# Performance work log

Measured on AMD Instinct MI355X. Metric: run time of the kernel, lower is better.

## Reference

```python
import jax, jax.numpy as jnp
import numpy as np

B, T, CIN, CH, SZ = 4, 6, 3, 64, 128
KS = [3, 5, 7]


def _conv(x, w, b, pad):
    # x: [N,Ci,H,W], w: [Co,Ci,k,k]
    y = jax.lax.conv_general_dilated(
        x, w, window_strides=(1, 1), padding=[(pad, pad), (pad, pad)],
        dimension_numbers=('NCHW', 'OIHW', 'NCHW'))
    return y + b[None, :, None, None]


def setup_inputs() -> dict:
    key = jax.random.key(0)
    ks = jax.random.split(key, 16)
    inp = {}
    inp['x'] = jax.random.normal(ks[0], (B, T, CIN, SZ, SZ), jnp.float32)
    for i in range(3):
        inp[f'h{i}'] = jnp.zeros((B, CH, SZ, SZ), jnp.float32)
    # 1x1 projection conv
    inp['w1x1'] = jax.random.normal(ks[1], (CH, CIN, 1, 1), jnp.float32) / np.sqrt(CIN).astype(np.float32)
    inp['b1x1'] = jnp.zeros((CH,), jnp.float32)
    # 3 ConvGRU layers, gates: reset (r), update (u), out (o)
    ki = 2
    for i, k in enumerate(KS):
        cin = (CIN if i == 0 else CH) + CH  # concat(input, hidden)
        s = np.float32(1.0 / np.sqrt(cin * k * k))
        for g in ('r', 'u', 'o'):
            inp[f'w{g}{i}'] = jax.random.normal(ks[ki], (CH, cin, k, k), jnp.float32) * s
            inp[f'b{g}{i}'] = jnp.zeros((CH,), jnp.float32)
            ki += 1
    return inp


def _cell(inp, h, wr, br, wu, bu, wo, bo, k):
    pad = k // 2
    stacked = jnp.concatenate([inp, h], axis=1)
    u = jax.nn.sigmoid(_conv(stacked, wu, bu, pad))
    r = jax.nn.sigmoid(_conv(stacked, wr, br, pad))
    o = jnp.tanh(_conv(jnp.concatenate([inp, h * r], axis=1), wo, bo, pad))
    return h * (1.0 - u) + o * u


def reference(x, h0, h1, h2, w1x1, b1x1,
              wr0, br0, wu0, bu0, wo0, bo0,
              wr1, br1, wu1, bu1, wo1, bo1,
              wr2, br2, wu2, bu2, wo2, bo2):
    b, t, c, hh, ww = x.shape
    x0 = _conv(x.reshape(b * t, c, hh, ww), w1x1, b1x1, 0)  # [b*t, CH, H, W]
    layers = [(wr0, br0, wu0, bu0, wo0, bo0, 3),
              (wr1, br1, wu1, bu1, wo1, bo1, 5),
              (wr2, br2, wu2, bu2, wo2, bo2, 7)]

    def step(carry, xt):
        hs = list(carry)
        layer_in = xt
        new_hs = []
        for i, (wr, br, wu, bu, wo, bo, k) in enumerate(layers):
            hn = _cell(layer_in, hs[i], wr, br, wu, bu, wo, bo, k)
            new_hs.append(hn)
            layer_in = hn
        return tuple(new_hs), None

    xs = jnp.transpose(x, (1, 0, 2, 3, 4))  # [t,b,c,H,W]
    (h0f, h1f, h2f), _ = jax.lax.scan(step, (h0, h1, h2), xs)
    # original returns ((x0, hidden[-1]), hidden); flattened here
    return (x0, h0f, h1f, h2f)
```

## Files before the change

### kernel.cpp

```cpp
#include <hip/hip_runtime.h>
#include <math.h>

constexpr int Bn  = 4;
constexpr int T   = 6;
constexpr int CIN = 3;
constexpr int CH  = 64;
constexpr int IMG = 128;
constexpr int HW  = IMG * IMG;

constexpr int CLY = 136;
constexpr long CLN = 4L * CLY * CLY * 64;
constexpr long CLNX = 4L * CLY * CLY * 32;

typedef short bf16x8 __attribute__((ext_vector_type(8)));
typedef float f32x4  __attribute__((ext_vector_type(4)));

__device__ __forceinline__ unsigned short f2bf(float f) {
    union { float f; unsigned int u; } v; v.f = f;
    unsigned int u = v.u;
    unsigned int r = (u + 0x7FFFu + ((u >> 16) & 1u)) >> 16;
    return (unsigned short)r;
}
__device__ __forceinline__ float bf2f(unsigned short s) {
    union { unsigned int u; float f; } v; v.u = ((unsigned int)s) << 16;
    return v.f;
}
__device__ __forceinline__ float sigmoidf_(float v) { return 1.f / (1.f + __expf(-v)); }
__device__ __forceinline__ float tanhf_(float v)    { return 1.f - 2.f / (1.f + __expf(2.f * v)); }

__global__ void xform_w(const float* __restrict__ wA, const float* __restrict__ wB,
                        unsigned short* __restrict__ dst,
                        int K, int C0, int NCIC, int NG) {
    int idx   = blockIdx.x * 256 + threadIdx.x;
    int total = NG * K * K * NCIC * 4 * 64;
    if (idx >= total) return;
    int CI   = C0 + 64;
    int KK   = K * K;
    int lane = idx & 63;
    int rest = idx >> 6;
    int c    = rest & 3; rest >>= 2;
    int cic  = rest % NCIC; rest /= NCIC;
    int kyx  = rest % KK;
    int cog  = rest / KK;
    const float* w = cog ? wB : wA;
    int co = c * 16 + (lane & 15);
    union { unsigned short u[8]; uint4 q; } t;
    #pragma unroll
    for (int j = 0; j < 8; ++j) {
        int ci_new = cic * 32 + ((lane >> 4) * 8) + j;
        int ci_o   = (ci_new < 64) ? (C0 + ci_new) : (ci_new - 64);
        bool valid = (ci_new < 64) || (ci_new - 64 < C0);
        float f = valid ? w[((long)co * CI + ci_o) * KK + kyx] : 0.f;
        t.u[j] = f2bf(f);
    }
    *(uint4*)(dst + (long)(idx >> 6) * 8 * 64 + lane * 8) = t.q;
}

__global__ void build_cl(const float* __restrict__ src, long bstride, int C0,
                         unsigned short* __restrict__ dst, int NG, int CST) {
    int i    = blockIdx.x * 256 + threadIdx.x;
    int px   = i & 16383;
    int rest = i >> 14;
    int g    = rest % NG;
    int b    = rest / NG;
    int y    = px >> 7, x = px & 127;
    union { unsigned short u[8]; uint4 q; } t;
    #pragma unroll
    for (int j = 0; j < 8; ++j) {
        int ci  = g * 8 + j;
        float f = (ci < C0) ? src[(long)b * bstride + (long)ci * HW + px] : 0.f;
        t.u[j] = f2bf(f);
    }
    long off = (((long)b * CLY + 4 + y) * CLY + 4 + x) * CST + g * 8;
    *(uint4*)(dst + off) = t.q;
}

__global__ void unpack_h(const unsigned short* __restrict__ clh, float* __restrict__ H) {
    int i  = blockIdx.x * 256 + threadIdx.x;
    int b  = i >> 14, px = i & 16383;
    int y  = px >> 7, x = px & 127;
    const unsigned short* p = clh + (((long)b * CLY + 4 + y) * CLY + 4 + x) * 64;
    float* Hb = H + (long)b * 64 * HW + px;
    #pragma unroll
    for (int g = 0; g < 8; ++g) {
        union { unsigned short us[8]; uint4 q; } t;
        t.q = *(const uint4*)(p + g * 8);
        #pragma unroll
        for (int j = 0; j < 8; ++j)
            Hb[(long)(g * 8 + j) * HW] = bf2f(t.us[j]);
    }
}

template<int K, int NCIC, int S, int MODE, int CST>
__global__ __launch_bounds__(256)
void conv_l0(const unsigned short* __restrict__ clh,
             const unsigned short* __restrict__ clin,
             const unsigned short* __restrict__ wt,
             const float* __restrict__ bias_a,
             const float* __restrict__ bias_b,
             unsigned short* __restrict__ ubuf,
             unsigned short* __restrict__ clh2,
             unsigned short* __restrict__ clhL)
{
    constexpr int HOFF = 4 - K / 2;
    constexpr int KK   = K * K;
    constexpr int NF   = NCIC * 4;
    __shared__ unsigned short alds[2][NF * 512];

    int w    = threadIdx.x >> 6;
    int lane = threadIdx.x & 63;
    int cog  = (MODE == 0) ? blockIdx.y : 0;
    int m    = blockIdx.x;
    int k8   = m & 7;
    int q    = m >> 3;
    int b    = k8 >> 1;
    int y, x0;
    if (S == 4) { y = (k8 & 1) * 64 + (q >> 1) * 4 + w; x0 = (q & 1) * 64; }
    else        { y = (k8 & 1) * 64 + (q >> 2) * 4 + w; x0 = (q & 3) * 32; }
    int n  = lane & 15;
    int kg = lane >> 4;

    f32x4 acc[4][S];
    #pragma unroll
    for (int c = 0; c < 4; ++c)
        #pragma unroll
        for (int s = 0; s < S; ++s)
            acc[c][s] = (f32x4){0.f, 0.f, 0.f, 0.f};

    long rbh = ((long)(b * CLY + HOFF + y) * CLY + HOFF + x0 + n) * 64 + kg * 8;
    long rbi = ((long)(b * CLY + HOFF + y) * CLY + HOFF + x0 + n) * CST + kg * 8;
    const unsigned short* wcog = wt + (long)cog * KK * NF * 512;

    #define STAGEW(bi, kyx_) do {                                              \
        const unsigned short* _src = wcog + (long)(kyx_) * NF * 512;           \
        _Pragma("unroll")                                                      \
        for (int j = 0; j < NCIC; ++j) {                                       \
            int f = j * 4 + w;                                                 \
            __builtin_amdgcn_global_load_lds(                                  \
                (const __attribute__((address_space(1))) void*)(_src + f * 512 + lane * 8), \
                (__attribute__((address_space(3))) void*)(&alds[bi][f * 512]), \
                16, 0, 0);                                                     \
        }                                                                      \
    } while (0)

    STAGEW(0, 0);
    int cur = 0;
    for (int kyx = 0; kyx < KK; ++kyx) {
        if (kyx + 1 < KK) {
            STAGEW(cur ^ 1, kyx + 1);
            asm volatile("s_waitcnt vmcnt(%0)" :: "n"(NCIC) : "memory");
        } else {
            asm volatile("s_waitcnt vmcnt(0)" ::: "memory");
        }
        __builtin_amdgcn_s_barrier();
        asm volatile("" ::: "memory");

        int ky = kyx / K;
        int kx = kyx - ky * K;
        long offh = rbh + (long)(ky * CLY + kx) * 64;
        long offi = rbi + (long)(ky * CLY + kx) * CST;
        #pragma unroll
        for (int cic = 0; cic < NCIC; ++cic) {
            bf16x8 bfr[S], afr[4];
            #pragma unroll
            for (int s = 0; s < S; ++s) {
                if (cic < 2) bfr[s] = *(const bf16x8*)(clh  + offh + s * 16 * 64  + cic * 32);
                else         bfr[s] = *(const bf16x8*)(clin + offi + s * 16 * CST + (cic - 2) * 32);
            }
            #pragma unroll
            for (int c = 0; c < 4; ++c)
                afr[c] = *(const bf16x8*)(&alds[cur][(cic * 4 + c) * 512 + lane * 8]);
            #pragma unroll
            for (int c = 0; c < 4; ++c)
                #pragma unroll
                for (int s = 0; s < S; ++s)
                    acc[c][s] = __builtin_amdgcn_mfma_f32_16x16x32_bf16(afr[c], bfr[s], acc[c][s], 0, 0, 0);
        }
        asm volatile("" ::: "memory");
        __builtin_amdgcn_s_barrier();
        cur ^= 1;
    }
    #undef STAGEW

    #pragma unroll
    for (int coc = 0; coc < 4; ++coc) {
        int co_l = coc * 16 + kg * 4;
        #pragma unroll
        for (int s = 0; s < S; ++s) {
            int x = x0 + s * 16 + n;
            f32x4 v = acc[coc][s];
            long cloff = (((long)b * CLY + 4 + y) * CLY + 4 + x) * 64 + co_l;
            if (MODE == 0) {
                if (cog == 0) {
                    union { unsigned short us[4]; unsigned long long d; } t;
                    #pragma unroll
                    for (int rr = 0; rr < 4; ++rr)
                        t.us[rr] = f2bf(sigmoidf_(v[rr] + bias_a[co_l + rr]));
                    *(unsigned long long*)(ubuf + (((long)b * HW + y * IMG + x) * 64 + co_l)) = t.d;
                } else {
                    union { unsigned short us[4]; unsigned long long d; } hh, t;
                    hh.d = *(const unsigned long long*)(clh + cloff);
                    #pragma unroll
                    for (int rr = 0; rr < 4; ++rr) {
                        float rv = sigmoidf_(v[rr] + bias_b[co_l + rr]);
                        t.us[rr] = f2bf(bf2f(hh.us[rr]) * rv);
                    }
                    *(unsigned long long*)(clh2 + cloff) = t.d;
                }
            } else {
                union { unsigned short us[4]; unsigned long long d; } uu, hh, t;
                uu.d = *(const unsigned long long*)(ubuf + (((long)b * HW + y * IMG + x) * 64 + co_l));
                hh.d = *(const unsigned long long*)(clhL + cloff);
                #pragma unroll
                for (int rr = 0; rr < 4; ++rr) {
                    float o  = tanhf_(v[rr] + bias_a[co_l + rr]);
                    float hv = bf2f(hh.us[rr]);
                    float uv = bf2f(uu.us[rr]);
                    t.us[rr] = f2bf(hv + uv * (o - hv));
                }
                *(unsigned long long*)(clhL + cloff) = t.d;
            }
        }
    }
}

template<int K, int MODE>
__global__ __launch_bounds__(512, 4)
void conv_db(const unsigned short* __restrict__ clh,
             const unsigned short* __restrict__ clin,
             const unsigned short* __restrict__ wt,
             const float* __restrict__ bias_a,
             const float* __restrict__ bias_b,
             unsigned short* __restrict__ ubuf,
             unsigned short* __restrict__ clh2,
             unsigned short* __restrict__ clhL)
{
    constexpr int HOFF = 4 - K / 2;
    constexpr int KK   = K * K;
    constexpr int ROWS = K + 3;
    constexpr int PXT  = 31 + K;
    constexpr int SUBT = ROWS * PXT;
    constexpr int SUBTP = (SUBT + 7) & ~7;
    constexpr int NCHUNK = 4 * SUBTP;
    constexpr int NGRP = NCHUNK / 64;
    constexpr int VCNT = NGRP / 8;
    constexpr int NCW = (MODE == 0) ? 2 : 1;
    constexpr int D   = 4;

    __shared__ __align__(16) unsigned char tile[2][NCHUNK * 16];

    int tid  = threadIdx.x;
    int w    = tid >> 6;
    int lane = tid & 63;
    int cog  = (MODE == 0) ? (w >> 2) : 0;
    int cb   = (MODE == 0) ? ((w >> 1) & 1) * 2 : (w >> 1);
    int rp   = w & 1;
    int m    = blockIdx.x;
    int k8   = m & 7;
    int t8   = m >> 3;
    int b    = k8 >> 1;
    int y0   = (k8 & 1) * 64 + (t8 >> 2) * 4;
    int x0   = (t8 & 3) * 32;
    int n    = lane & 15;
    int kg   = lane >> 4;

    f32x4 acc[NCW][2][2];
    #pragma unroll
    for (int c = 0; c < NCW; ++c)
        #pragma unroll
        for (int rr = 0; rr < 2; ++rr)
            #pragma unroll
            for (int s = 0; s < 2; ++s)
                acc[c][rr][s] = (f32x4){0.f, 0.f, 0.f, 0.f};

    const unsigned short* wbase = wt + (long)cog * KK * 16 * 512;

    #define STAGE(bi, ph_) do {                                                \
        const unsigned short* sp_ = ((ph_) < 2) ? clh : clin;                  \
        int half_ = ((ph_) & 1) * 32;                                          \
        _Pragma("unroll 1")                                                    \
        for (int g = w; g < NGRP; g += 8) {                                    \
            int c_  = g * 64 + lane;                                           \
            int cg  = c_ / SUBTP;                                              \
            int rem = c_ - cg * SUBTP;                                         \
            int r   = rem / PXT;                                               \
            int px  = rem - r * PXT;                                           \
            const unsigned short* src_ = sp_ +                                 \
                (((long)(b * CLY + HOFF + y0 + r)) * CLY + (HOFF + x0 + px)) * 64 \
                + half_ + cg * 8;                                              \
            __builtin_amdgcn_global_load_lds(                                  \
                (const __attribute__((address_space(1))) void*)src_,           \
                (__attribute__((address_space(3))) void*)(&tile[bi][g * 64 * 16]), \
                16, 0, 0);                                                     \
        }                                                                      \
    } while (0)

    int cur = 0;
    STAGE(0, 0);
    #pragma unroll 1
    for (int ph = 0; ph < 4; ++ph) {
        if (ph < 3) {
            STAGE(cur ^ 1, ph + 1);
            asm volatile("s_waitcnt vmcnt(%0)" :: "n"(VCNT) : "memory");
        } else {
            asm volatile("s_waitcnt vmcnt(0)" ::: "memory");
        }
        __builtin_amdgcn_s_barrier();
        asm volatile("" ::: "memory");

        const unsigned char* tb = tile[cur];
        const unsigned short* wph = wbase + (long)(4 * ph + cb) * 512 + lane * 8;

        bf16x8 apre[D][NCW];
        #pragma unroll
        for (int tt = 0; tt < D; ++tt)
            #pragma unroll
            for (int c = 0; c < NCW; ++c)
                apre[tt][c] = *(const bf16x8*)(wph + (long)tt * 8192 + c * 512);

        #pragma unroll
        for (int t = 0; t < KK; ++t) {
            constexpr int PXB = PXT * 16;
            int slot = t % D;
            bf16x8 aC[NCW];
            #pragma unroll
            for (int c = 0; c < NCW; ++c) aC[c] = apre[slot][c];
            if (t + D < KK) {
                #pragma unroll
                for (int c = 0; c < NCW; ++c)
                    apre[slot][c] = *(const bf16x8*)(wph + (long)(t + D) * 8192 + c * 512);
            }
            int ky = t / K, kx = t - (t / K) * K;
            const unsigned char* row0 = tb + (kg * SUBTP + (rp * 2 + 0 + ky) * PXT) * 16;
            const unsigned char* row1 = row0 + PXB;
            bf16x8 bv[2][2];
            #pragma unroll
            for (int s = 0; s < 2; ++s) {
                bv[0][s] = *(const bf16x8*)(row0 + (kx + s * 16 + n) * 16);
                bv[1][s] = *(const bf16x8*)(row1 + (kx + s * 16 + n) * 16);
            }
            #pragma unroll
            for (int c = 0; c < NCW; ++c)
                #pragma unroll
                for (int rr = 0; rr < 2; ++rr)
                    #pragma unroll
                    for (int s = 0; s < 2; ++s)
                        acc[c][rr][s] = __builtin_amdgcn_mfma_f32_16x16x32_bf16(aC[c], bv[rr][s], acc[c][rr][s], 0, 0, 0);
        }
        asm volatile("" ::: "memory");
        __builtin_amdgcn_s_barrier();
        cur ^= 1;
    }
    #undef STAGE

    #pragma unroll
    for (int c = 0; c < NCW; ++c) {
        int co_l = (cb + c) * 16 + kg * 4;
        #pragma unroll
        for (int rr = 0; rr < 2; ++rr) {
            int yy = y0 + rp * 2 + rr;
            #pragma unroll
            for (int s = 0; s < 2; ++s) {
                int xx = x0 + s * 16 + n;
                f32x4 v = acc[c][rr][s];
                long cloff = (((long)b * CLY + 4 + yy) * CLY + 4 + xx) * 64 + co_l;
                if (MODE == 0) {
                    if (cog == 0) {
                        union { unsigned short us[4]; unsigned long long d; } t;
                        #pragma unroll
                        for (int q4 = 0; q4 < 4; ++q4)
                            t.us[q4] = f2bf(sigmoidf_(v[q4] + bias_a[co_l + q4]));
                        *(unsigned long long*)(ubuf + (((long)b * HW + yy * IMG + xx) * 64 + co_l)) = t.d;
                    } else {
                        union { unsigned short us[4]; unsigned long long d; } hh, t;
                        hh.d = *(const unsigned long long*)(clh + cloff);
                        #pragma unroll
                        for (int q4 = 0; q4 < 4; ++q4) {
                            float rv = sigmoidf_(v[q4] + bias_b[co_l + q4]);
                            t.us[q4] = f2bf(bf2f(hh.us[q4]) * rv);
                        }
                        *(unsigned long long*)(clh2 + cloff) = t.d;
                    }
                } else {
                    union { unsigned short us[4]; unsigned long long d; } uu, hh, t;
                    uu.d = *(const unsigned long long*)(ubuf + (((long)b * HW + yy * IMG + xx) * 64 + co_l));
                    hh.d = *(const unsigned long long*)(clhL + cloff);
                    #pragma unroll
                    for (int q4 = 0; q4 < 4; ++q4) {
                        float o  = tanhf_(v[q4] + bias_a[co_l + q4]);
                        float hv = bf2f(hh.us[q4]);
                        float uv = bf2f(uu.us[q4]);
                        t.us[q4] = f2bf(hv + uv * (o - hv));
                    }
                    *(unsigned long long*)(clhL + cloff) = t.d;
                }
            }
        }
    }
}

__global__ void conv1x1(const float* __restrict__ x, const float* __restrict__ w,
                        const float* __restrict__ bias, float* __restrict__ out) {
    int i  = blockIdx.x * 256 + threadIdx.x;
    int q  = HW / 4;
    int p4 = i % q;
    int co = (i / q) & 63;
    int f  = i / (q * 64);
    const float4* xb = reinterpret_cast<const float4*>(x + (long)f * 3 * HW);
    float4 x0 = xb[p4];
    float4 x1 = xb[p4 + q];
    float4 x2 = xb[p4 + 2 * q];
    float w0 = w[co * 3], w1 = w[co * 3 + 1], w2 = w[co * 3 + 2];
    float bv = bias[co];
    float4 o;
    o.x = bv + x0.x * w0 + x1.x * w1 + x2.x * w2;
    o.y = bv + x0.y * w0 + x1.y * w1 + x2.y * w2;
    o.z = bv + x0.z * w0 + x1.z * w1 + x2.z * w2;
    o.w = bv + x0.w * w0 + x1.w * w1 + x2.w * w2;
    reinterpret_cast<float4*>(out)[i] = o;
}

extern "C" void kernel_launch(void* const* d_in, const int* in_sizes, int n_in,
                              void* d_out, int out_size, void* d_ws, size_t ws_size,
                              hipStream_t stream) {
    (void)in_sizes; (void)n_in; (void)out_size; (void)d_ws; (void)ws_size;

    const float* x  = (const float*)d_in[0];
    const float* w1 = (const float*)d_in[4];
    const float* b1 = (const float*)d_in[5];

    float* out = (float*)d_out;

    const long X0_N = 24L * CH * HW;
    const long HN   = (long)Bn * CH * HW;

    float* H[3] = { out + X0_N, out + X0_N + HN, out + X0_N + 2 * HN };

    unsigned short* sc    = (unsigned short*)out;
    unsigned short* ubuf  = sc;
    unsigned short* CLH0  = sc + 4194304;
    unsigned short* CLH1  = CLH0 + CLN;
    unsigned short* CLH2  = CLH1 + CLN;
    unsigned short* clh2  = CLH2 + CLN;
    unsigned short* clinx = clh2 + CLN;
    unsigned short* wt    = clinx + CLNX;

    const long WT_UR[3] = { 0,      165888, 780288  };
    const long WT_O [3] = { 110592, 575488, 1583104 };

    const int Ks[3]   = { 3, 5, 7 };
    const int C0s[3]  = { CIN, CH, CH };
    const int NCIC[3] = { 3, 4, 4 };

    hipMemsetAsync(CLH0, 0, (4 * CLN + CLNX) * sizeof(unsigned short), stream);

    for (int L = 0; L < 3; ++L) {
        const float* wr = (const float*)d_in[6 + 6 * L];
        const float* wu = (const float*)d_in[8 + 6 * L];
        const float* wo = (const float*)d_in[10 + 6 * L];
        int K = Ks[L], C0 = C0s[L], NC = NCIC[L];
        int tot_ur = 2 * K * K * NC * 4 * 64;
        int tot_o  = 1 * K * K * NC * 4 * 64;
        xform_w<<<(tot_ur + 255) / 256, 256, 0, stream>>>(wu, wr, wt + WT_UR[L], K, C0, NC, 2);
        xform_w<<<(tot_o  + 255) / 256, 256, 0, stream>>>(wo, wo, wt + WT_O[L],  K, C0, NC, 1);
    }

    unsigned short* CLH[3] = { CLH0, CLH1, CLH2 };
    for (int L = 0; L < 3; ++L)
        build_cl<<<4 * 8 * 64, 256, 0, stream>>>((const float*)d_in[1 + L],
                                                 (long)CH * HW, 64, CLH[L], 8, 64);

    for (int t = 0; t < T; ++t) {
        build_cl<<<4 * 4 * 64, 256, 0, stream>>>(x + (long)t * CIN * HW,
                                                 (long)T * CIN * HW, CIN, clinx, 4, 32);
        {
            const float* br = (const float*)d_in[7];
            const float* bu = (const float*)d_in[9];
            const float* bo = (const float*)d_in[11];
            conv_l0<3, 3, 4, 0, 32><<<dim3(256, 2), 256, 0, stream>>>(
                CLH0, clinx, wt + WT_UR[0], bu, br, ubuf, clh2, nullptr);
            conv_l0<3, 3, 2, 1, 32><<<dim3(512, 1), 256, 0, stream>>>(
                clh2, clinx, wt + WT_O[0], bo, nullptr, ubuf, nullptr, CLH0);
        }
        {
            const float* br = (const float*)d_in[13];
            const float* bu = (const float*)d_in[15];
            const float* bo = (const float*)d_in[17];
            conv_db<5, 0><<<512, 512, 0, stream>>>(
                CLH1, CLH0, wt + WT_UR[1], bu, br, ubuf, clh2, nullptr);
            conv_db<5, 1><<<512, 512, 0, stream>>>(
                clh2, CLH0, wt + WT_O[1], bo, nullptr, ubuf, nullptr, CLH1);
        }
        {
            const float* br = (const float*)d_in[19];
            const float* bu = (const float*)d_in[21];
            const float* bo = (const float*)d_in[23];
            conv_db<7, 0><<<512, 512, 0, stream>>>(
                CLH2, CLH1, wt + WT_UR[2], bu, br, ubuf, clh2, nullptr);
            conv_db<7, 1><<<512, 512, 0, stream>>>(
                clh2, CLH1, wt + WT_O[2], bo, nullptr, ubuf, nullptr, CLH2);
        }
    }

    for (int L = 0; L < 3; ++L)
        unpack_h<<<256, 256, 0, stream>>>(CLH[L], H[L]);

    conv1x1<<<(24 * CH * HW / 4 + 255) / 256, 256, 0, stream>>>(x, w1, b1, out);
}
```

Measured before the change: 1.851 ms.

## Generalize conv_db for layer 0 and halve MODE 1 block to 256 threads

Removes the separate conv_l0 kernel and runs layer 0 through the LDS-tiled conv_db kernel. conv_db gains template parameters for the number of input phases and the input channel stride, so layer 0's narrower 32-channel input buffer can be handled. The output-gate kernel (MODE 1) now launches 4 waves per block instead of 8, with each wave covering two output-channel chunks. The aim is to reuse activation tiles staged in LDS for layer 0 and to lower per-block overhead for the o-gate; the trade-offs are more registers per wave and fewer waves sharing the staging work in MODE 1.

```diff
diff --git a/kernel.cpp b/kernel.cpp
--- a/kernel.cpp
+++ b/kernel.cpp
@@ -91,140 +91,7 @@
     }
 }
 
-template<int K, int NCIC, int S, int MODE, int CST>
-__global__ __launch_bounds__(256)
-void conv_l0(const unsigned short* __restrict__ clh,
-             const unsigned short* __restrict__ clin,
-             const unsigned short* __restrict__ wt,
-             const float* __restrict__ bias_a,
-             const float* __restrict__ bias_b,
-             unsigned short* __restrict__ ubuf,
-             unsigned short* __restrict__ clh2,
-             unsigned short* __restrict__ clhL)
-{
-    constexpr int HOFF = 4 - K / 2;
-    constexpr int KK   = K * K;
-    constexpr int NF   = NCIC * 4;
-    __shared__ unsigned short alds[2][NF * 512];
-
-    int w    = threadIdx.x >> 6;
-    int lane = threadIdx.x & 63;
-    int cog  = (MODE == 0) ? blockIdx.y : 0;
-    int m    = blockIdx.x;
-    int k8   = m & 7;
-    int q    = m >> 3;
-    int b    = k8 >> 1;
-    int y, x0;
-    if (S == 4) { y = (k8 & 1) * 64 + (q >> 1) * 4 + w; x0 = (q & 1) * 64; }
-    else        { y = (k8 & 1) * 64 + (q >> 2) * 4 + w; x0 = (q & 3) * 32; }
-    int n  = lane & 15;
-    int kg = lane >> 4;
-
-    f32x4 acc[4][S];
-    #pragma unroll
-    for (int c = 0; c < 4; ++c)
-        #pragma unroll
-        for (int s = 0; s < S; ++s)
-            acc[c][s] = (f32x4){0.f, 0.f, 0.f, 0.f};
-
-    long rbh = ((long)(b * CLY + HOFF + y) * CLY + HOFF + x0 + n) * 64 + kg * 8;
-    long rbi = ((long)(b * CLY + HOFF + y) * CLY + HOFF + x0 + n) * CST + kg * 8;
-    const unsigned short* wcog = wt + (long)cog * KK * NF * 512;
-
-    #define STAGEW(bi, kyx_) do {                                              \
-        const unsigned short* _src = wcog + (long)(kyx_) * NF * 512;           \
-        _Pragma("unroll")                                                      \
-        for (int j = 0; j < NCIC; ++j) {                                       \
-            int f = j * 4 + w;                                                 \
-            __builtin_amdgcn_global_load_lds(                                  \
-                (const __attribute__((address_space(1))) void*)(_src + f * 512 + lane * 8), \
-                (__attribute__((address_space(3))) void*)(&alds[bi][f * 512]), \
-                16, 0, 0);                                                     \
-        }                                                                      \
-    } while (0)
-
-    STAGEW(0, 0);
-    int cur = 0;
-    for (int kyx = 0; kyx < KK; ++kyx) {
-        if (kyx + 1 < KK) {
-            STAGEW(cur ^ 1, kyx + 1);
-            asm volatile("s_waitcnt vmcnt(%0)" :: "n"(NCIC) : "memory");
-        } else {
-            asm volatile("s_waitcnt vmcnt(0)" ::: "memory");
-        }
-        __builtin_amdgcn_s_barrier();
-        asm volatile("" ::: "memory");
-
-        int ky = kyx / K;
-        int kx = kyx - ky * K;
-        long offh = rbh + (long)(ky * CLY + kx) * 64;
-        long offi = rbi + (long)(ky * CLY + kx) * CST;
-        #pragma unroll
-        for (int cic = 0; cic < NCIC; ++cic) {
-            bf16x8 bfr[S], afr[4];
-            #pragma unroll
-            for (int s = 0; s < S; ++s) {
-                if (cic < 2) bfr[s] = *(const bf16x8*)(clh  + offh + s * 16 * 64  + cic * 32);
-                else         bfr[s] = *(const bf16x8*)(clin + offi + s * 16 * CST + (cic - 2) * 32);
-            }
-            #pragma unroll
-            for (int c = 0; c < 4; ++c)
-                afr[c] = *(const bf16x8*)(&alds[cur][(cic * 4 + c) * 512 + lane * 8]);
-            #pragma unroll
-            for (int c = 0; c < 4; ++c)
-                #pragma unroll
-                for (int s = 0; s < S; ++s)
-                    acc[c][s] = __builtin_amdgcn_mfma_f32_16x16x32_bf16(afr[c], bfr[s], acc[c][s], 0, 0, 0);
-        }
-        asm volatile("" ::: "memory");
-        __builtin_amdgcn_s_barrier();
-        cur ^= 1;
-    }
-    #undef STAGEW
-
-    #pragma unroll
-    for (int coc = 0; coc < 4; ++coc) {
-        int co_l = coc * 16 + kg * 4;
-        #pragma unroll
-        for (int s = 0; s < S; ++s) {
-            int x = x0 + s * 16 + n;
-            f32x4 v = acc[coc][s];
-            long cloff = (((long)b * CLY + 4 + y) * CLY + 4 + x) * 64 + co_l;
-            if (MODE == 0) {
-                if (cog == 0) {
-                    union { unsigned short us[4]; unsigned long long d; } t;
-                    #pragma unroll
-                    for (int rr = 0; rr < 4; ++rr)
-                        t.us[rr] = f2bf(sigmoidf_(v[rr] + bias_a[co_l + rr]));
-                    *(unsigned long long*)(ubuf + (((long)b * HW + y * IMG + x) * 64 + co_l)) = t.d;
-                } else {
-                    union { unsigned short us[4]; unsigned long long d; } hh, t;
-                    hh.d = *(const unsigned long long*)(clh + cloff);
-                    #pragma unroll
-                    for (int rr = 0; rr < 4; ++rr) {
-                        float rv = sigmoidf_(v[rr] + bias_b[co_l + rr]);
-                        t.us[rr] = f2bf(bf2f(hh.us[rr]) * rv);
-                    }
-                    *(unsigned long long*)(clh2 + cloff) = t.d;
-                }
-            } else {
-                union { unsigned short us[4]; unsigned long long d; } uu, hh, t;
-                uu.d = *(const unsigned long long*)(ubuf + (((long)b * HW + y * IMG + x) * 64 + co_l));
-                hh.d = *(const unsigned long long*)(clhL + cloff);
-                #pragma unroll
-                for (int rr = 0; rr < 4; ++rr) {
-                    float o  = tanhf_(v[rr] + bias_a[co_l + rr]);
-                    float hv = bf2f(hh.us[rr]);
-                    float uv = bf2f(uu.us[rr]);
-                    t.us[rr] = f2bf(hv + uv * (o - hv));
-                }
-                *(unsigned long long*)(clhL + cloff) = t.d;
-            }
-        }
-    }
-}
-
-template<int K, int MODE>
+template<int K, int MODE, int NPH, int CSTIN>
 __global__ __launch_bounds__(512, 4)
 void conv_db(const unsigned short* __restrict__ clh,
              const unsigned short* __restrict__ clin,
@@ -243,18 +110,20 @@
     constexpr int SUBTP = (SUBT + 7) & ~7;
     constexpr int NCHUNK = 4 * SUBTP;
     constexpr int NGRP = NCHUNK / 64;
-    constexpr int VCNT = NGRP / 8;
-    constexpr int NCW = (MODE == 0) ? 2 : 1;
-    constexpr int D   = 4;
+    constexpr int NW   = (MODE == 0) ? 8 : 4;
+    constexpr int VCNT = NGRP / NW;
+    constexpr int NCW  = 2;
+    constexpr int D    = 4;
+    constexpr long TAPSTR = (long)NPH * 2048;
 
     __shared__ __align__(16) unsigned char tile[2][NCHUNK * 16];
 
     int tid  = threadIdx.x;
     int w    = tid >> 6;
     int lane = tid & 63;
-    int cog  = (MODE == 0) ? (w >> 2) : 0;
-    int cb   = (MODE == 0) ? ((w >> 1) & 1) * 2 : (w >> 1);
-    int rp   = w & 1;
+    int cog, cb, rp;
+    if (MODE == 0) { cog = w >> 2; cb = ((w >> 1) & 1) * 2; rp = w & 1; }
+    else           { cog = 0;      cb = (w >> 1) * 2;       rp = w & 1; }
     int m    = blockIdx.x;
     int k8   = m & 7;
     int t8   = m >> 3;
@@ -273,20 +142,21 @@
             for (int s = 0; s < 2; ++s)
                 acc[c][rr][s] = (f32x4){0.f, 0.f, 0.f, 0.f};
 
-    const unsigned short* wbase = wt + (long)cog * KK * 16 * 512;
+    const unsigned short* wbase = wt + (long)cog * KK * TAPSTR;
 
     #define STAGE(bi, ph_) do {                                                \
-        const unsigned short* sp_ = ((ph_) < 2) ? clh : clin;                  \
-        int half_ = ((ph_) & 1) * 32;                                          \
+        const unsigned short* sp_; int cst_, half_;                            \
+        if ((ph_) < 2) { sp_ = clh; cst_ = 64; half_ = ((ph_) & 1) * 32; }     \
+        else { sp_ = clin; cst_ = CSTIN; half_ = (((ph_) - 2) & 1) * 32; }     \
         _Pragma("unroll 1")                                                    \
-        for (int g = w; g < NGRP; g += 8) {                                    \
+        for (int g = w; g < NGRP; g += NW) {                                   \
             int c_  = g * 64 + lane;                                           \
             int cg  = c_ / SUBTP;                                              \
             int rem = c_ - cg * SUBTP;                                         \
             int r   = rem / PXT;                                               \
             int px  = rem - r * PXT;                                           \
             const unsigned short* src_ = sp_ +                                 \
-                (((long)(b * CLY + HOFF + y0 + r)) * CLY + (HOFF + x0 + px)) * 64 \
+                (((long)(b * CLY + HOFF + y0 + r)) * CLY + (HOFF + x0 + px)) * cst_ \
                 + half_ + cg * 8;                                              \
             __builtin_amdgcn_global_load_lds(                                  \
                 (const __attribute__((address_space(1))) void*)src_,           \
@@ -298,8 +168,8 @@
     int cur = 0;
     STAGE(0, 0);
     #pragma unroll 1
-    for (int ph = 0; ph < 4; ++ph) {
-        if (ph < 3) {
+    for (int ph = 0; ph < NPH; ++ph) {
+        if (ph < NPH - 1) {
             STAGE(cur ^ 1, ph + 1);
             asm volatile("s_waitcnt vmcnt(%0)" :: "n"(VCNT) : "memory");
         } else {
@@ -316,7 +186,7 @@
         for (int tt = 0; tt < D; ++tt)
             #pragma unroll
             for (int c = 0; c < NCW; ++c)
-                apre[tt][c] = *(const bf16x8*)(wph + (long)tt * 8192 + c * 512);
+                apre[tt][c] = *(const bf16x8*)(wph + (long)tt * TAPSTR + c * 512);
 
         #pragma unroll
         for (int t = 0; t < KK; ++t) {
@@ -328,7 +198,7 @@
             if (t + D < KK) {
                 #pragma unroll
                 for (int c = 0; c < NCW; ++c)
-                    apre[slot][c] = *(const bf16x8*)(wph + (long)(t + D) * 8192 + c * 512);
+                    apre[slot][c] = *(const bf16x8*)(wph + (long)(t + D) * TAPSTR + c * 512);
             }
             int ky = t / K, kx = t - (t / K) * K;
             const unsigned char* row0 = tb + (kg * SUBTP + (rp * 2 + 0 + ky) * PXT) * 16;
@@ -477,27 +347,27 @@
             const float* br = (const float*)d_in[7];
             const float* bu = (const float*)d_in[9];
             const float* bo = (const float*)d_in[11];
-            conv_l0<3, 3, 4, 0, 32><<<dim3(256, 2), 256, 0, stream>>>(
+            conv_db<3, 0, 3, 32><<<512, 512, 0, stream>>>(
                 CLH0, clinx, wt + WT_UR[0], bu, br, ubuf, clh2, nullptr);
-            conv_l0<3, 3, 2, 1, 32><<<dim3(512, 1), 256, 0, stream>>>(
+            conv_db<3, 1, 3, 32><<<512, 256, 0, stream>>>(
                 clh2, clinx, wt + WT_O[0], bo, nullptr, ubuf, nullptr, CLH0);
         }
         {
             const float* br = (const float*)d_in[13];
             const float* bu = (const float*)d_in[15];
             const float* bo = (const float*)d_in[17];
-            conv_db<5, 0><<<512, 512, 0, stream>>>(
+            conv_db<5, 0, 4, 64><<<512, 512, 0, stream>>>(
                 CLH1, CLH0, wt + WT_UR[1], bu, br, ubuf, clh2, nullptr);
-            conv_db<5, 1><<<512, 512, 0, stream>>>(
+            conv_db<5, 1, 4, 64><<<512, 256, 0, stream>>>(
                 clh2, CLH0, wt + WT_O[1], bo, nullptr, ubuf, nullptr, CLH1);
         }
         {
             const float* br = (const float*)d_in[19];
             const float* bu = (const float*)d_in[21];
             const float* bo = (const float*)d_in[23];
-            conv_db<7, 0><<<512, 512, 0, stream>>>(
+            conv_db<7, 0, 4, 64><<<512, 512, 0, stream>>>(
                 CLH2, CLH1, wt + WT_UR[2], bu, br, ubuf, clh2, nullptr);
-            conv_db<7, 1><<<512, 512, 0, stream>>>(
+            conv_db<7, 1, 4, 64><<<512, 256, 0, stream>>>(
                 clh2, CLH1, wt + WT_O[2], bo, nullptr, ubuf, nullptr, CLH2);
         }
     }
```

Result: no change. 1.882 ms (+1.7%).
